# Optimization experiments

Hardware: AMD Instinct MI355X
Metric: run time of the kernel (lower is better)

The kernel has to match this reference:

```python
import jax, jax.numpy as jnp
import numpy as np

# Model dims (from SsmTransformerDecoderLayer defaults)
DM = 256      # d_model
H = 8         # nheads
EXPAND = 2
DI = EXPAND * DM   # d_inner = 512
P = DI // H        # headdim = 64
G = 1              # ngroups
ND = 16            # d_dist
N = 300            # d_state = num_proposal = Q
EPS_RMS = 1e-5
EPS_LN = 1e-5


def _init_params():
    rng = np.random.default_rng(0)
    # dt_bias init as in the module
    dt0 = np.exp(rng.uniform(size=H) * (np.log(0.1) - np.log(1e-4)) + np.log(1e-4))
    dt0 = np.clip(dt0, 1e-4, None)
    inv_dt = dt0 + np.log(-np.expm1(-dt0))
    A0 = rng.uniform(1.0, 16.0, size=H)
    return jnp.asarray(inv_dt, jnp.float32), jnp.asarray(np.log(A0), jnp.float32)


def setup_inputs() -> dict:
    key = jax.random.key(0)
    ks = jax.random.split(key, 12)
    B, L, Q = 2, 2048, N
    d_in_key = 2 * DI + 2 * G + H  # 1034
    s = 0.02
    dt_bias, A_log = _init_params()
    return {
        "in_key": jax.random.normal(ks[0], (B, L, DM), jnp.float32),
        "in_query": jax.random.normal(ks[1], (B, Q, DM), jnp.float32),
        "dist": jax.random.normal(ks[2], (B, L, Q, ND), jnp.float32),
        "W_key": jax.random.normal(ks[3], (d_in_key, DM), jnp.float32) * s,
        "W_query": jax.random.normal(ks[4], (DI, DM), jnp.float32) * s,
        "W_bc": jax.random.normal(ks[5], (2 * G, ND), jnp.float32) * s,
        "W_dt": jax.random.normal(ks[6], (H, ND), jnp.float32) * s,
        "dt_bias": dt_bias,
        "A_log": A_log,
        "D": jnp.ones((H,), jnp.float32),
        "W_out_key": jax.random.normal(ks[7], (DM, DI), jnp.float32) * s,
        "W_out_query": jax.random.normal(ks[8], (DM, DI), jnp.float32) * s,
        "key_norm_w": jnp.ones((DI,), jnp.float32),
        "q_norm_w": jnp.ones((DI,), jnp.float32),
        "q_norm_b": jnp.zeros((DI,), jnp.float32),
    }


def _selective_scan(x4, dt, Bm, Cm, init, A, D):
    """ISSM selective scan.
    x4 [B,L,H,P], dt [B,L,H,N] (per-query dt!), Bm/Cm [B,L,G=1,N],
    init [B,H,P,N], A [H], D [H].
    Returns y [B,L,H,P], last state [B,H,P,N].
    """
    def step(S, inp):
        xt, dtt, Bt, Ct = inp  # [B,H,P], [B,H,N], [B,1,N], [B,1,N]
        dA = jnp.exp(dtt * A[None, :, None])                    # [B,H,N]
        S = S * dA[:, :, None, :] + (dtt * Bt)[:, :, None, :] * xt[..., None]
        y = jnp.einsum('bhpn,bn->bhp', S, Ct[:, 0])
        return S, y
    xs = (jnp.moveaxis(x4, 1, 0), jnp.moveaxis(dt, 1, 0),
          jnp.moveaxis(Bm, 1, 0), jnp.moveaxis(Cm, 1, 0))
    S_last, ys = jax.lax.scan(step, init, xs)
    y = jnp.moveaxis(ys, 0, 1) + x4 * D[None, None, :, None]   # D skip
    return y, S_last


def reference(in_key, in_query, dist, W_key, W_query, W_bc, W_dt, dt_bias,
              A_log, D, W_out_key, W_out_query, key_norm_w, q_norm_w, q_norm_b):
    Bsz, L, _ = in_key.shape
    Q = in_query.shape[1]
    # projections
    zxbcdt = in_key @ W_key.T                                   # [B,L,2*DI+2G+H]
    z, x, b_bias, c_bias, dtb = jnp.split(
        zxbcdt, [DI, 2 * DI, 2 * DI + G, 2 * DI + 2 * G], axis=-1)
    init = (in_query @ W_query.T).reshape(Bsz, Q, H, P).transpose(0, 2, 3, 1)  # [B,H,P,Q]
    A = -jnp.exp(A_log)                                         # [H]
    bc = dist @ W_bc.T                                          # [B,L,Q,2G]
    Bm = (bc[..., :G] + b_bias[:, :, None, :]).transpose(0, 1, 3, 2)  # [B,L,G,Q]
    Cm = (bc[..., G:] + c_bias[:, :, None, :]).transpose(0, 1, 3, 2)
    dt_base = (dist @ W_dt.T).transpose(0, 1, 3, 2)             # [B,L,H,Q]
    dt = jax.nn.softplus(dt_base + dtb[..., None] + dt_bias[None, None, :, None])
    x4 = x.reshape(Bsz, L, H, P)
    # forward scan
    y_f, S_f = _selective_scan(x4, dt, Bm, Cm, init, A, D)
    # backward scan (biscan): x_back/B_back/C_back are copies of forward, flipped
    flip = lambda t: jnp.flip(t, axis=1)
    y_b, S_b = _selective_scan(flip(x4), flip(dt), flip(Bm), flip(Cm), init, A, D)
    y = (y_f + flip(y_b)) * 0.5
    S = (S_f + S_b) * 0.5
    # gated RMSNorm on key (norm_before_gate=False: gate first, then norm)
    kf = y.reshape(Bsz, L, DI)
    g = kf * jax.nn.silu(z)
    kf = g * jax.lax.rsqrt(jnp.mean(g * g, axis=-1, keepdims=True) + EPS_RMS) * key_norm_w
    out_key = kf @ W_out_key.T
    # LayerNorm on final states
    last = S.transpose(0, 3, 1, 2).reshape(Bsz, Q, DI)          # b h d q -> b q (h d)
    mu = jnp.mean(last, axis=-1, keepdims=True)
    var = jnp.var(last, axis=-1, keepdims=True)
    lastn = (last - mu) * jax.lax.rsqrt(var + EPS_LN) * q_norm_w + q_norm_b
    out_query = lastn @ W_out_query.T
    return out_key, out_query
```

## Files before the change

### kernel.cpp

```cpp
#include <hip/hip_runtime.h>
#include <hip/hip_bf16.h>
#include <cstdio>

#define BS   2
#define LL   2048
#define HH   8
#define PP   64
#define NQ   300
#define NPAD 320
#define NG   5
#define PJ   8
#define TT   128
#define NCH  16
#define DI   512
#define DKEY 1034

__global__ __launch_bounds__(256) void gemm_nt(
    const float* __restrict__ A, const float* __restrict__ Bm, float* __restrict__ C,
    int M, int N, int K, int lda, int ldb, int ldc)
{
    __shared__ float As[16][68];
    __shared__ float Bs[16][68];
    const int tid = threadIdx.x;
    const int tx = tid & 15, ty = tid >> 4;
    const int m0 = blockIdx.x * 64, n0 = blockIdx.y * 64;
    const int lr = tid >> 2, lk = (tid & 3) << 2;
    float acc[4][4] = {};
    for (int k0 = 0; k0 < K; k0 += 16) {
        float4 av = make_float4(0.f,0.f,0.f,0.f), bv = make_float4(0.f,0.f,0.f,0.f);
        int am = m0 + lr;
        if (am < M) av = *(const float4*)(A + (size_t)am * lda + k0 + lk);
        int bn = n0 + lr;
        if (bn < N) bv = *(const float4*)(Bm + (size_t)bn * ldb + k0 + lk);
        __syncthreads();
        As[lk+0][lr] = av.x; As[lk+1][lr] = av.y; As[lk+2][lr] = av.z; As[lk+3][lr] = av.w;
        Bs[lk+0][lr] = bv.x; Bs[lk+1][lr] = bv.y; Bs[lk+2][lr] = bv.z; Bs[lk+3][lr] = bv.w;
        __syncthreads();
        #pragma unroll
        for (int kk = 0; kk < 16; ++kk) {
            float a0 = As[kk][ty*4+0], a1 = As[kk][ty*4+1], a2 = As[kk][ty*4+2], a3 = As[kk][ty*4+3];
            float b0 = Bs[kk][tx*4+0], b1 = Bs[kk][tx*4+1], b2 = Bs[kk][tx*4+2], b3 = Bs[kk][tx*4+3];
            acc[0][0] = fmaf(a0,b0,acc[0][0]); acc[0][1] = fmaf(a0,b1,acc[0][1]);
            acc[0][2] = fmaf(a0,b2,acc[0][2]); acc[0][3] = fmaf(a0,b3,acc[0][3]);
            acc[1][0] = fmaf(a1,b0,acc[1][0]); acc[1][1] = fmaf(a1,b1,acc[1][1]);
            acc[1][2] = fmaf(a1,b2,acc[1][2]); acc[1][3] = fmaf(a1,b3,acc[1][3]);
            acc[2][0] = fmaf(a2,b0,acc[2][0]); acc[2][1] = fmaf(a2,b1,acc[2][1]);
            acc[2][2] = fmaf(a2,b2,acc[2][2]); acc[2][3] = fmaf(a2,b3,acc[2][3]);
            acc[3][0] = fmaf(a3,b0,acc[3][0]); acc[3][1] = fmaf(a3,b1,acc[3][1]);
            acc[3][2] = fmaf(a3,b2,acc[3][2]); acc[3][3] = fmaf(a3,b3,acc[3][3]);
        }
    }
    #pragma unroll
    for (int i = 0; i < 4; ++i) {
        int m = m0 + ty*4 + i;
        if (m >= M) continue;
        #pragma unroll
        for (int j = 0; j < 4; ++j) {
            int n = n0 + tx*4 + j;
            if (n < N) C[(size_t)m * ldc + n] = acc[i][j];
        }
    }
}

__global__ __launch_bounds__(256) void gemm_nt_big(
    const float* __restrict__ A, const float* __restrict__ Bm, float* __restrict__ C,
    int M, int N, int K, int lda, int ldb, int ldc)
{
    __shared__ float As[16][132];
    __shared__ float Bs[16][68];
    const int tid = threadIdx.x;
    const int tx = tid & 15, ty = tid >> 4;
    const int m0 = blockIdx.x * 128, n0 = blockIdx.y * 64;
    const int lr = tid >> 2, lk = (tid & 3) << 2;
    float acc[8][4] = {};
    for (int k0 = 0; k0 < K; k0 += 16) {
        float4 a0v = make_float4(0.f,0.f,0.f,0.f), a1v = a0v, bv = a0v;
        int am0 = m0 + lr, am1 = m0 + 64 + lr;
        if (am0 < M) a0v = *(const float4*)(A + (size_t)am0 * lda + k0 + lk);
        if (am1 < M) a1v = *(const float4*)(A + (size_t)am1 * lda + k0 + lk);
        int bn = n0 + lr;
        if (bn < N) bv = *(const float4*)(Bm + (size_t)bn * ldb + k0 + lk);
        __syncthreads();
        As[lk+0][lr] = a0v.x; As[lk+1][lr] = a0v.y; As[lk+2][lr] = a0v.z; As[lk+3][lr] = a0v.w;
        As[lk+0][64+lr] = a1v.x; As[lk+1][64+lr] = a1v.y; As[lk+2][64+lr] = a1v.z; As[lk+3][64+lr] = a1v.w;
        Bs[lk+0][lr] = bv.x; Bs[lk+1][lr] = bv.y; Bs[lk+2][lr] = bv.z; Bs[lk+3][lr] = bv.w;
        __syncthreads();
        #pragma unroll
        for (int kk = 0; kk < 16; ++kk) {
            float a[8], b[4];
            #pragma unroll
            for (int i = 0; i < 8; ++i) a[i] = As[kk][ty*8+i];
            #pragma unroll
            for (int j = 0; j < 4; ++j) b[j] = Bs[kk][tx*4+j];
            #pragma unroll
            for (int i = 0; i < 8; ++i)
                #pragma unroll
                for (int j = 0; j < 4; ++j)
                    acc[i][j] = fmaf(a[i], b[j], acc[i][j]);
        }
    }
    #pragma unroll
    for (int i = 0; i < 8; ++i) {
        int m = m0 + ty*8 + i;
        if (m >= M) continue;
        #pragma unroll
        for (int j = 0; j < 4; ++j) {
            int n = n0 + tx*4 + j;
            if (n < N) C[(size_t)m * ldc + n] = acc[i][j];
        }
    }
}

__global__ __launch_bounds__(256) void dtbc_kernel(
    const float* __restrict__ dist, const float* __restrict__ zx,
    const float* __restrict__ W_bc, const float* __restrict__ W_dt,
    const float* __restrict__ dt_bias, const float* __restrict__ A_log,
    float2* __restrict__ pairs, float* __restrict__ Cc)
{
    const int r = blockIdx.x;
    const int b = r >> 11, l = r & 2047;
    const int tid = threadIdx.x;
    const float bb = zx[(size_t)r*DKEY + 1024];
    const float cb = zx[(size_t)r*DKEY + 1025];
    #pragma unroll
    for (int rep = 0; rep < 2; ++rep) {
        int n = rep*256 + tid;
        if (n >= NPAD) continue;
        if (n < NQ) {
            const float4* dp = (const float4*)(dist + ((size_t)r*NQ + n)*16);
            float d[16];
            #pragma unroll
            for (int j = 0; j < 4; ++j) {
                float4 v = dp[j];
                d[4*j+0]=v.x; d[4*j+1]=v.y; d[4*j+2]=v.z; d[4*j+3]=v.w;
            }
            float Bv = bb, Cv = cb;
            #pragma unroll
            for (int j = 0; j < 16; ++j) {
                Bv = fmaf(d[j], W_bc[j],     Bv);
                Cv = fmaf(d[j], W_bc[16+j],  Cv);
            }
            Cc[(size_t)r*NPAD + n] = Cv;
            #pragma unroll
            for (int h = 0; h < HH; ++h) {
                float s = zx[(size_t)r*DKEY + 1026 + h] + dt_bias[h];
                #pragma unroll
                for (int j = 0; j < 16; ++j) s = fmaf(d[j], W_dt[h*16+j], s);
                float dtv = (s > 20.f) ? s : log1pf(expf(s));
                float Ah = -expf(A_log[h]);
                pairs[((size_t)(b*HH+h)*LL + l)*NPAD + n] = make_float2(expf(dtv*Ah), dtv*Bv);
            }
        } else {
            Cc[(size_t)r*NPAD + n] = 0.f;
            #pragma unroll
            for (int h = 0; h < HH; ++h)
                pairs[((size_t)(b*HH+h)*LL + l)*NPAD + n] = make_float2(1.f, 0.f);
        }
    }
}

__global__ __launch_bounds__(320) void adec_kernel(
    const float2* __restrict__ pairs, float* __restrict__ Adec4)
{
    const int bid = blockIdx.x;
    const int q = bid & 3, c = (bid >> 2) & 15, bh = bid >> 6;
    const int n = threadIdx.x;
    const float2* pr = pairs + ((size_t)bh*LL + c*TT + q*32)*NPAD + n;
    float prod = 1.f;
    #pragma unroll 8
    for (int t = 0; t < 32; ++t) prod *= pr[(size_t)t*NPAD].x;
    Adec4[(((size_t)bh*NCH + c)*4 + q)*NPAD + n] = prod;
}

__global__ __launch_bounds__(320) void transpose_proj(
    const float* __restrict__ proj, float* __restrict__ projT)
{
    const int bid = blockIdx.x;
    const int p = bid & 63, h = (bid >> 6) & 7, b = bid >> 9;
    const int n = threadIdx.x;
    float v = 0.f;
    if (n < NQ) v = proj[((size_t)(b*NQ + n))*DI + h*64 + p];
    projT[(size_t)bid*NPAD + n] = v;
}

__device__ __forceinline__ float reduce8x64(const float yl[8], int L)
{
    const bool h1 = (L & 1), h2 = (L & 2), h4 = (L & 4);
    float t0 = (h1 ? yl[1] : yl[0]) + __shfl_xor(h1 ? yl[0] : yl[1], 1, 64);
    float t1 = (h1 ? yl[3] : yl[2]) + __shfl_xor(h1 ? yl[2] : yl[3], 1, 64);
    float t2 = (h1 ? yl[5] : yl[4]) + __shfl_xor(h1 ? yl[4] : yl[5], 1, 64);
    float t3 = (h1 ? yl[7] : yl[6]) + __shfl_xor(h1 ? yl[6] : yl[7], 1, 64);
    float u0 = (h2 ? t1 : t0) + __shfl_xor(h2 ? t0 : t1, 2, 64);
    float u1 = (h2 ? t3 : t2) + __shfl_xor(h2 ? t2 : t3, 2, 64);
    float v  = (h4 ? u1 : u0) + __shfl_xor(h4 ? u0 : u1, 4, 64);
    v += __shfl_xor(v, 8, 64);
    v += __shfl_xor(v, 16, 64);
    v += __shfl_xor(v, 32, 64);
    return v;
}

__global__ __launch_bounds__(512, 4) void sweepA(
    const float2* __restrict__ pairs, const float* __restrict__ Cc,
    const float* __restrict__ zx,
    float* __restrict__ Sloc, float* __restrict__ yFa, float* __restrict__ yBa)
{
    const int bid = blockIdx.x;
    const int c = bid & 15, h = (bid >> 4) & 7, b = (bid >> 7) & 1, dir = bid >> 8;
    const int tid = threadIdx.x;
    const int L = tid & 63, w = tid >> 6;
    float* __restrict__ ybuf = dir ? yBa : yFa;

    __shared__ float xs[TT*64];

    for (int idx = tid; idx < TT*64; idx += 512) {
        int t = idx >> 6, pp = idx & 63;
        int ls = c*TT + t;
        int l = dir ? (LL-1-ls) : ls;
        xs[idx] = zx[(size_t)(b*LL + l)*DKEY + 512 + h*64 + pp];
    }
    __syncthreads();

    const int lstart = dir ? (LL-1 - c*TT) : c*TT;
    const int lstep  = dir ? -1 : 1;
    const float2* __restrict__ pb = pairs + ((size_t)(b*HH+h)*LL + lstart)*NPAD + L;
    const float*  __restrict__ cb = Cc + ((size_t)(b*LL) + lstart)*NPAD + L;
    const ptrdiff_t pstride = (ptrdiff_t)lstep * NPAD;

    float S[NG][PJ];
    #pragma unroll
    for (int g = 0; g < NG; ++g)
        #pragma unroll
        for (int j = 0; j < PJ; ++j) S[g][j] = 0.f;

    float2 pv[2][NG]; float cv[2][NG];
    #pragma unroll
    for (int g = 0; g < NG; ++g) { pv[0][g] = pb[g*64]; cv[0][g] = cb[g*64]; }

    for (int t8 = 0; t8 < TT/8; ++t8) {
        #pragma unroll
        for (int tt = 0; tt < 8; ++tt) {
            const int t = t8*8 + tt;
            const int cur = tt & 1, nxt = cur ^ 1;
            const int tn = (t+1 < TT) ? t+1 : t;
            const float2* pn = pb + (ptrdiff_t)tn * pstride;
            const float*  cn = cb + (ptrdiff_t)tn * pstride;
            #pragma unroll
            for (int g = 0; g < NG; ++g) { pv[nxt][g] = pn[g*64]; cv[nxt][g] = cn[g*64]; }

            const float4* xp = (const float4*)&xs[(t << 6) + w*PJ];
            float4 xa = xp[0], xb2 = xp[1];
            float xv[8] = {xa.x, xa.y, xa.z, xa.w, xb2.x, xb2.y, xb2.z, xb2.w};

            float yl[8];
            #pragma unroll
            for (int j = 0; j < 8; ++j) yl[j] = 0.f;
            #pragma unroll
            for (int g = 0; g < NG; ++g) {
                const float a = pv[cur][g].x, u = pv[cur][g].y, cg = cv[cur][g];
                #pragma unroll
                for (int j = 0; j < PJ; ++j) {
                    S[g][j] = fmaf(S[g][j], a, u * xv[j]);
                    yl[j] = fmaf(S[g][j], cg, yl[j]);
                }
            }
            float v = reduce8x64(yl, L);
            if (L < 8) {
                int l = lstart + t*lstep;
                ybuf[(((size_t)(b*LL + l))*HH + h)*64 + w*PJ + L] = v;
            }
        }
    }
    const int dbh = dir*16 + b*8 + h;
    const size_t sb = (((size_t)dbh*NCH + c)*64)*NPAD;
    #pragma unroll
    for (int g = 0; g < NG; ++g)
        #pragma unroll
        for (int j = 0; j < PJ; ++j)
            Sloc[sb + (size_t)(w*PJ + j)*NPAD + g*64 + L] = S[g][j];
}

__global__ __launch_bounds__(320) void chunkscan(
    const float* __restrict__ Sloc, const float* __restrict__ Adec4,
    const float* __restrict__ projT, float* __restrict__ carry)
{
    const int bid = blockIdx.x;
    const int p = bid & 63, dbh = bid >> 6;
    const int bh = dbh & 15, dir = dbh >> 4;
    const int n = threadIdx.x;
    float cur = projT[(size_t)(bh*64 + p)*NPAD + n];
    carry[((size_t)(dbh*(NCH+1) + 0)*64 + p)*NPAD + n] = cur;
    #pragma unroll
    for (int cc = 0; cc < NCH; ++cc) {
        int cF = dir ? (NCH-1-cc) : cc;
        const float* a4 = Adec4 + ((size_t)(bh*NCH + cF)*4)*NPAD + n;
        float ad = a4[0]*a4[NPAD]*a4[2*NPAD]*a4[3*NPAD];
        cur = fmaf(cur, ad, Sloc[((size_t)(dbh*NCH + cc)*64 + p)*NPAD + n]);
        carry[((size_t)(dbh*(NCH+1) + cc + 1)*64 + p)*NPAD + n] = cur;
    }
}

__global__ __launch_bounds__(512, 4) void sweepB(
    const float2* __restrict__ pairs, const float* __restrict__ Cc,
    const float* __restrict__ carry,
    float* __restrict__ yFb, float* __restrict__ yBb)
{
    const int bid = blockIdx.x;
    const int c = bid & 15, h = (bid >> 4) & 7, b = (bid >> 7) & 1, dir = bid >> 8;
    const int tid = threadIdx.x;
    const int L = tid & 63, w = tid >> 6;
    float* __restrict__ ybuf = dir ? yBb : yFb;

    const int dbh = dir*16 + b*8 + h;
    const size_t cb0 = ((size_t)(dbh*(NCH+1) + c)*64)*NPAD;
    float cr[NG][PJ];
    #pragma unroll
    for (int g = 0; g < NG; ++g)
        #pragma unroll
        for (int j = 0; j < PJ; ++j)
            cr[g][j] = carry[cb0 + (size_t)(w*PJ + j)*NPAD + g*64 + L];

    const int lstart = dir ? (LL-1 - c*TT) : c*TT;
    const int lstep  = dir ? -1 : 1;
    const float2* __restrict__ pb = pairs + ((size_t)(b*HH+h)*LL + lstart)*NPAD + L;
    const float*  __restrict__ cb = Cc + ((size_t)(b*LL) + lstart)*NPAD + L;
    const ptrdiff_t pstride = (ptrdiff_t)lstep * NPAD;

    float2 pv[2][NG]; float cv[2][NG];
    #pragma unroll
    for (int g = 0; g < NG; ++g) { pv[0][g] = pb[g*64]; cv[0][g] = cb[g*64]; }

    for (int t8 = 0; t8 < TT/8; ++t8) {
        #pragma unroll
        for (int tt = 0; tt < 8; ++tt) {
            const int t = t8*8 + tt;
            const int cur = tt & 1, nxt = cur ^ 1;
            const int tn = (t+1 < TT) ? t+1 : t;
            const float2* pn = pb + (ptrdiff_t)tn * pstride;
            const float*  cn = cb + (ptrdiff_t)tn * pstride;
            #pragma unroll
            for (int g = 0; g < NG; ++g) { pv[nxt][g] = pn[g*64]; cv[nxt][g] = cn[g*64]; }

            float yl[8];
            #pragma unroll
            for (int j = 0; j < 8; ++j) yl[j] = 0.f;
            #pragma unroll
            for (int g = 0; g < NG; ++g) {
                const float a = pv[cur][g].x, cg = cv[cur][g];
                #pragma unroll
                for (int j = 0; j < PJ; ++j) {
                    cr[g][j] *= a;
                    yl[j] = fmaf(cr[g][j], cg, yl[j]);
                }
            }
            float v = reduce8x64(yl, L);
            if (L < 8) {
                int l = lstart + t*lstep;
                ybuf[(((size_t)(b*LL + l))*HH + h)*64 + w*PJ + L] = v;
            }
        }
    }
}

__global__ __launch_bounds__(256) void gate_rms(
    const float* __restrict__ zx,
    const float* __restrict__ yFa, const float* __restrict__ yBa,
    const float* __restrict__ yFb, const float* __restrict__ yBb,
    const float* __restrict__ Dp,
    const float* __restrict__ knw, float* __restrict__ kfn)
{
    const int r = blockIdx.x, tid = threadIdx.x;
    __shared__ float part[4];
    float g[2];
    #pragma unroll
    for (int rep = 0; rep < 2; ++rep) {
        int dcol = rep*256 + tid;
        size_t yi = (size_t)r*DI + dcol;
        float zv = zx[(size_t)r*DKEY + dcol];
        float xv = zx[(size_t)r*DKEY + 512 + dcol];
        float yv = 0.5f*(yFa[yi] + yBa[yi] + yFb[yi] + yBb[yi]) + xv * Dp[dcol >> 6];
        float sig = 1.f / (1.f + expf(-zv));
        g[rep] = yv * (zv * sig);
    }
    float ss = g[0]*g[0] + g[1]*g[1];
    #pragma unroll
    for (int o = 32; o; o >>= 1) ss += __shfl_xor(ss, o, 64);
    if ((tid & 63) == 0) part[tid >> 6] = ss;
    __syncthreads();
    float tot = part[0] + part[1] + part[2] + part[3];
    float scale = rsqrtf(tot * (1.f/512.f) + 1e-5f);
    #pragma unroll
    for (int rep = 0; rep < 2; ++rep) {
        int dcol = rep*256 + tid;
        kfn[(size_t)r*DI + dcol] = g[rep] * scale * knw[dcol];
    }
}

__global__ __launch_bounds__(512) void state_ln(
    const float* __restrict__ carry, const float* __restrict__ qw,
    const float* __restrict__ qb, float* __restrict__ lastn)
{
    const int row = blockIdx.x;
    const int b = row / NQ, q = row % NQ;
    const int tid = threadIdx.x;
    const int h = tid >> 6, p = tid & 63;
    __shared__ float pm[8], pv[8];
    size_t iF = ((size_t)((0*16 + b*8 + h)*(NCH+1) + NCH)*64 + p)*NPAD + q;
    size_t iB = ((size_t)((16   + b*8 + h)*(NCH+1) + NCH)*64 + p)*NPAD + q;
    float v = 0.5f * (carry[iF] + carry[iB]);
    float s1 = v, s2 = v*v;
    #pragma unroll
    for (int o = 32; o; o >>= 1) { s1 += __shfl_xor(s1, o, 64); s2 += __shfl_xor(s2, o, 64); }
    if ((tid & 63) == 0) { pm[tid >> 6] = s1; pv[tid >> 6] = s2; }
    __syncthreads();
    float m = 0.f, s = 0.f;
    #pragma unroll
    for (int i = 0; i < 8; ++i) { m += pm[i]; s += pv[i]; }
    m *= (1.f/512.f);
    s = s*(1.f/512.f) - m*m;
    lastn[(size_t)row*DI + tid] = (v - m)*rsqrtf(s + 1e-5f)*qw[tid] + qb[tid];
}

extern "C" void kernel_launch(void* const* d_in, const int* in_sizes, int n_in,
                              void* d_out, int out_size, void* d_ws, size_t ws_size,
                              hipStream_t stream)
{
    const float* in_key    = (const float*)d_in[0];
    const float* in_query  = (const float*)d_in[1];
    const float* dist      = (const float*)d_in[2];
    const float* W_key     = (const float*)d_in[3];
    const float* W_query   = (const float*)d_in[4];
    const float* W_bc      = (const float*)d_in[5];
    const float* W_dt      = (const float*)d_in[6];
    const float* dt_bias   = (const float*)d_in[7];
    const float* A_log     = (const float*)d_in[8];
    const float* Dp        = (const float*)d_in[9];
    const float* W_out_key = (const float*)d_in[10];
    const float* W_out_qry = (const float*)d_in[11];
    const float* knw       = (const float*)d_in[12];
    const float* qw        = (const float*)d_in[13];
    const float* qb        = (const float*)d_in[14];
    float* out = (float*)d_out;

    float* ws = (float*)d_ws;
    size_t off = 0;
    auto alloc = [&](size_t nf) { float* pp = ws + off; off += nf; return pp; };
    float*  zx    = alloc((size_t)4096*DKEY);
    float*  proj  = alloc((size_t)600*DI);
    float*  projT = alloc((size_t)1024*NPAD);
    float2* pairs = (float2*)alloc((size_t)16*LL*NPAD*2);
    float*  Cc    = alloc((size_t)BS*LL*NPAD);
    float*  Sloc  = alloc((size_t)32*NCH*64*NPAD);
    float*  Adec4 = alloc((size_t)16*NCH*4*NPAD);
    float*  carry = alloc((size_t)32*(NCH+1)*64*NPAD);
    float*  yFa   = alloc((size_t)BS*LL*DI);
    float*  yBa   = alloc((size_t)BS*LL*DI);
    float*  yFb   = Sloc;
    float*  yBb   = Sloc + (size_t)BS*LL*DI;
    float*  kfn   = Sloc + (size_t)2*BS*LL*DI;
    float*  lastn = Sloc + (size_t)3*BS*LL*DI;
    if (off * sizeof(float) > ws_size) {
        fprintf(stderr, "kernel_launch: workspace too small: need %zu bytes, have %zu\n",
                off * sizeof(float), ws_size);
        return;
    }

    dim3 blk(256);
    gemm_nt_big<<<dim3(32, 17), blk, 0, stream>>>(in_key, W_key, zx, 4096, DKEY, 256, 256, 256, DKEY);
    gemm_nt<<<dim3(10, 8), blk, 0, stream>>>(in_query, W_query, proj, 600, DI, 256, 256, 256, DI);
    transpose_proj<<<1024, dim3(320), 0, stream>>>(proj, projT);
    dtbc_kernel<<<4096, blk, 0, stream>>>(dist, zx, W_bc, W_dt, dt_bias, A_log, pairs, Cc);
    adec_kernel<<<1024, dim3(320), 0, stream>>>(pairs, Adec4);
    sweepA<<<512, dim3(512), 0, stream>>>(pairs, Cc, zx, Sloc, yFa, yBa);
    chunkscan<<<2048, dim3(320), 0, stream>>>(Sloc, Adec4, projT, carry);
    sweepB<<<512, dim3(512), 0, stream>>>(pairs, Cc, carry, yFb, yBb);
    gate_rms<<<4096, blk, 0, stream>>>(zx, yFa, yBa, yFb, yBb, Dp, knw, kfn);
    gemm_nt<<<dim3(64, 4), blk, 0, stream>>>(kfn, W_out_key, out, 4096, 256, DI, DI, DI, 256);
    state_ln<<<600, dim3(512), 0, stream>>>(carry, qw, qb, lastn);
    gemm_nt<<<dim3(10, 4), blk, 0, stream>>>(lastn, W_out_qry, out + (size_t)4096*256, 600, 256, DI, DI, DI, 256);
}
```

Before: 591.6 us.

## Halve scan chunk length, overwrite Sloc with carries in place, accumulate sweepB into yA

Chunk length drops from 128 to 64, so there are 32 chunks and twice as many blocks in sweepA and sweepB for more parallelism. The chunk scan now writes each incoming carry over Sloc in place and stores only the final state, which removes the separate carry buffer. sweepB adds its contribution into the sweepA y buffers with read-modify-write, so gate_rms reads two y arrays instead of four. The cost is twice as much per-chunk Sloc state traffic and a longer sequential chunkscan loop. kfn and lastn are moved into the Sloc region, which is safe because Sloc is finished with by the time they are written.

```diff
diff --git a/kernel.cpp b/kernel.cpp
--- a/kernel.cpp
+++ b/kernel.cpp
@@ -10,8 +10,8 @@
 #define NPAD 320
 #define NG   5
 #define PJ   8
-#define TT   128
-#define NCH  16
+#define TT   64
+#define NCH  32
 #define DI   512
 #define DKEY 1034
 
@@ -160,16 +160,16 @@
 }
 
 __global__ __launch_bounds__(320) void adec_kernel(
-    const float2* __restrict__ pairs, float* __restrict__ Adec4)
+    const float2* __restrict__ pairs, float* __restrict__ Adec)
 {
     const int bid = blockIdx.x;
-    const int q = bid & 3, c = (bid >> 2) & 15, bh = bid >> 6;
+    const int c = bid & (NCH-1), bh = bid >> 5;
     const int n = threadIdx.x;
-    const float2* pr = pairs + ((size_t)bh*LL + c*TT + q*32)*NPAD + n;
+    const float2* pr = pairs + ((size_t)bh*LL + c*TT)*NPAD + n;
     float prod = 1.f;
     #pragma unroll 8
-    for (int t = 0; t < 32; ++t) prod *= pr[(size_t)t*NPAD].x;
-    Adec4[(((size_t)bh*NCH + c)*4 + q)*NPAD + n] = prod;
+    for (int t = 0; t < TT; ++t) prod *= pr[(size_t)t*NPAD].x;
+    Adec[((size_t)bh*NCH + c)*NPAD + n] = prod;
 }
 
 __global__ __launch_bounds__(320) void transpose_proj(
@@ -205,7 +205,7 @@
     float* __restrict__ Sloc, float* __restrict__ yFa, float* __restrict__ yBa)
 {
     const int bid = blockIdx.x;
-    const int c = bid & 15, h = (bid >> 4) & 7, b = (bid >> 7) & 1, dir = bid >> 8;
+    const int c = bid & (NCH-1), h = (bid >> 5) & 7, b = (bid >> 8) & 1, dir = bid >> 9;
     const int tid = threadIdx.x;
     const int L = tid & 63, w = tid >> 6;
     float* __restrict__ ybuf = dir ? yBa : yFa;
@@ -280,44 +280,45 @@
 }
 
 __global__ __launch_bounds__(320) void chunkscan(
-    const float* __restrict__ Sloc, const float* __restrict__ Adec4,
-    const float* __restrict__ projT, float* __restrict__ carry)
+    float* __restrict__ Sloc, const float* __restrict__ Adec,
+    const float* __restrict__ projT, float* __restrict__ Sfin)
 {
     const int bid = blockIdx.x;
     const int p = bid & 63, dbh = bid >> 6;
     const int bh = dbh & 15, dir = dbh >> 4;
     const int n = threadIdx.x;
     float cur = projT[(size_t)(bh*64 + p)*NPAD + n];
-    carry[((size_t)(dbh*(NCH+1) + 0)*64 + p)*NPAD + n] = cur;
-    #pragma unroll
+    #pragma unroll 4
     for (int cc = 0; cc < NCH; ++cc) {
         int cF = dir ? (NCH-1-cc) : cc;
-        const float* a4 = Adec4 + ((size_t)(bh*NCH + cF)*4)*NPAD + n;
-        float ad = a4[0]*a4[NPAD]*a4[2*NPAD]*a4[3*NPAD];
-        cur = fmaf(cur, ad, Sloc[((size_t)(dbh*NCH + cc)*64 + p)*NPAD + n]);
-        carry[((size_t)(dbh*(NCH+1) + cc + 1)*64 + p)*NPAD + n] = cur;
-    }
+        float ad = Adec[((size_t)bh*NCH + cF)*NPAD + n];
+        size_t si = ((size_t)(dbh*NCH + cc)*64 + p)*NPAD + n;
+        float s = Sloc[si];
+        Sloc[si] = cur;
+        cur = fmaf(cur, ad, s);
+    }
+    Sfin[((size_t)dbh*64 + p)*NPAD + n] = cur;
 }
 
 __global__ __launch_bounds__(512, 4) void sweepB(
     const float2* __restrict__ pairs, const float* __restrict__ Cc,
-    const float* __restrict__ carry,
-    float* __restrict__ yFb, float* __restrict__ yBb)
+    const float* __restrict__ Sloc,
+    float* __restrict__ yFa, float* __restrict__ yBa)
 {
     const int bid = blockIdx.x;
-    const int c = bid & 15, h = (bid >> 4) & 7, b = (bid >> 7) & 1, dir = bid >> 8;
+    const int c = bid & (NCH-1), h = (bid >> 5) & 7, b = (bid >> 8) & 1, dir = bid >> 9;
     const int tid = threadIdx.x;
     const int L = tid & 63, w = tid >> 6;
-    float* __restrict__ ybuf = dir ? yBb : yFb;
+    float* __restrict__ ybuf = dir ? yBa : yFa;
 
     const int dbh = dir*16 + b*8 + h;
-    const size_t cb0 = ((size_t)(dbh*(NCH+1) + c)*64)*NPAD;
+    const size_t cb0 = (((size_t)dbh*NCH + c)*64)*NPAD;
     float cr[NG][PJ];
     #pragma unroll
     for (int g = 0; g < NG; ++g)
         #pragma unroll
         for (int j = 0; j < PJ; ++j)
-            cr[g][j] = carry[cb0 + (size_t)(w*PJ + j)*NPAD + g*64 + L];
+            cr[g][j] = Sloc[cb0 + (size_t)(w*PJ + j)*NPAD + g*64 + L];
 
     const int lstart = dir ? (LL-1 - c*TT) : c*TT;
     const int lstep  = dir ? -1 : 1;
@@ -355,7 +356,8 @@
             float v = reduce8x64(yl, L);
             if (L < 8) {
                 int l = lstart + t*lstep;
-                ybuf[(((size_t)(b*LL + l))*HH + h)*64 + w*PJ + L] = v;
+                size_t yi = (((size_t)(b*LL + l))*HH + h)*64 + w*PJ + L;
+                ybuf[yi] += v;
             }
         }
     }
@@ -364,7 +366,6 @@
 __global__ __launch_bounds__(256) void gate_rms(
     const float* __restrict__ zx,
     const float* __restrict__ yFa, const float* __restrict__ yBa,
-    const float* __restrict__ yFb, const float* __restrict__ yBb,
     const float* __restrict__ Dp,
     const float* __restrict__ knw, float* __restrict__ kfn)
 {
@@ -377,7 +378,7 @@
         size_t yi = (size_t)r*DI + dcol;
         float zv = zx[(size_t)r*DKEY + dcol];
         float xv = zx[(size_t)r*DKEY + 512 + dcol];
-        float yv = 0.5f*(yFa[yi] + yBa[yi] + yFb[yi] + yBb[yi]) + xv * Dp[dcol >> 6];
+        float yv = 0.5f*(yFa[yi] + yBa[yi]) + xv * Dp[dcol >> 6];
         float sig = 1.f / (1.f + expf(-zv));
         g[rep] = yv * (zv * sig);
     }
@@ -396,7 +397,7 @@
 }
 
 __global__ __launch_bounds__(512) void state_ln(
-    const float* __restrict__ carry, const float* __restrict__ qw,
+    const float* __restrict__ Sfin, const float* __restrict__ qw,
     const float* __restrict__ qb, float* __restrict__ lastn)
 {
     const int row = blockIdx.x;
@@ -404,9 +405,9 @@
     const int tid = threadIdx.x;
     const int h = tid >> 6, p = tid & 63;
     __shared__ float pm[8], pv[8];
-    size_t iF = ((size_t)((0*16 + b*8 + h)*(NCH+1) + NCH)*64 + p)*NPAD + q;
-    size_t iB = ((size_t)((16   + b*8 + h)*(NCH+1) + NCH)*64 + p)*NPAD + q;
-    float v = 0.5f * (carry[iF] + carry[iB]);
+    size_t iF = ((size_t)((b*8 + h)*64) + p)*NPAD + q;
+    size_t iB = ((size_t)((16 + b*8 + h)*64) + p)*NPAD + q;
+    float v = 0.5f * (Sfin[iF] + Sfin[iB]);
     float s1 = v, s2 = v*v;
     #pragma unroll
     for (int o = 32; o; o >>= 1) { s1 += __shfl_xor(s1, o, 64); s2 += __shfl_xor(s2, o, 64); }
@@ -450,14 +451,12 @@
     float2* pairs = (float2*)alloc((size_t)16*LL*NPAD*2);
     float*  Cc    = alloc((size_t)BS*LL*NPAD);
     float*  Sloc  = alloc((size_t)32*NCH*64*NPAD);
-    float*  Adec4 = alloc((size_t)16*NCH*4*NPAD);
-    float*  carry = alloc((size_t)32*(NCH+1)*64*NPAD);
+    float*  Adec  = alloc((size_t)16*NCH*NPAD);
+    float*  Sfin  = alloc((size_t)32*64*NPAD);
     float*  yFa   = alloc((size_t)BS*LL*DI);
     float*  yBa   = alloc((size_t)BS*LL*DI);
-    float*  yFb   = Sloc;
-    float*  yBb   = Sloc + (size_t)BS*LL*DI;
-    float*  kfn   = Sloc + (size_t)2*BS*LL*DI;
-    float*  lastn = Sloc + (size_t)3*BS*LL*DI;
+    float*  kfn   = Sloc;
+    float*  lastn = Sloc + (size_t)4096*DI;
     if (off * sizeof(float) > ws_size) {
         fprintf(stderr, "kernel_launch: workspace too small: need %zu bytes, have %zu\n",
                 off * sizeof(float), ws_size);
@@ -469,12 +468,12 @@
     gemm_nt<<<dim3(10, 8), blk, 0, stream>>>(in_query, W_query, proj, 600, DI, 256, 256, 256, DI);
     transpose_proj<<<1024, dim3(320), 0, stream>>>(proj, projT);
     dtbc_kernel<<<4096, blk, 0, stream>>>(dist, zx, W_bc, W_dt, dt_bias, A_log, pairs, Cc);
-    adec_kernel<<<1024, dim3(320), 0, stream>>>(pairs, Adec4);
-    sweepA<<<512, dim3(512), 0, stream>>>(pairs, Cc, zx, Sloc, yFa, yBa);
-    chunkscan<<<2048, dim3(320), 0, stream>>>(Sloc, Adec4, projT, carry);
-    sweepB<<<512, dim3(512), 0, stream>>>(pairs, Cc, carry, yFb, yBb);
-    gate_rms<<<4096, blk, 0, stream>>>(zx, yFa, yBa, yFb, yBb, Dp, knw, kfn);
+    adec_kernel<<<512, dim3(320), 0, stream>>>(pairs, Adec);
+    sweepA<<<1024, dim3(512), 0, stream>>>(pairs, Cc, zx, Sloc, yFa, yBa);
+    chunkscan<<<2048, dim3(320), 0, stream>>>(Sloc, Adec, projT, Sfin);
+    sweepB<<<1024, dim3(512), 0, stream>>>(pairs, Cc, Sloc, yFa, yBa);
+    gate_rms<<<4096, blk, 0, stream>>>(zx, yFa, yBa, Dp, knw, kfn);
     gemm_nt<<<dim3(64, 4), blk, 0, stream>>>(kfn, W_out_key, out, 4096, 256, DI, DI, DI, 256);
-    state_ln<<<600, dim3(512), 0, stream>>>(carry, qw, qb, lastn);
+    state_ln<<<600, dim3(512), 0, stream>>>(Sfin, qw, qb, lastn);
     gemm_nt<<<dim3(10, 4), blk, 0, stream>>>(lastn, W_out_qry, out + (size_t)4096*256, 600, 256, DI, DI, DI, 256);
 }
```

New measurement: 610.4 us. 3.2% more time.
